# Kernel optimization log

Hardware: AMD Instinct MI355X
Metric: run time of the kernel (lower is better)

Reference implementation:

```python
import jax, jax.numpy as jnp
import numpy as np


def setup_inputs() -> dict:
    key = jax.random.key(0)
    k1, k2 = jax.random.split(key)
    pred = jax.random.normal(k1, (4, 8192, 3), dtype=jnp.float32)
    label = jax.random.normal(k2, (4, 8192, 3), dtype=jnp.float32)
    return {"pred": pred, "label": label}


def reference(pred, label):
    # Pairwise Euclidean distances via the Gram-matrix identity
    # explicit repeat+subtract+norm, without the [B,N,M,D] blowup).
    x2 = jnp.sum(pred * pred, axis=-1)            # [B, N]
    y2 = jnp.sum(label * label, axis=-1)          # [B, M]
    xy = jnp.einsum('bnd,bmd->bnm', pred, label)  # [B, N, M]
    d2 = x2[:, :, None] + y2[:, None, :] - 2.0 * xy
    dis = jnp.sqrt(jnp.maximum(d2, 0.0))          # [B, N, M]
    dis_xy = jnp.mean(jnp.min(dis, axis=2))       # pred -> nearest label
    dis_yx = jnp.mean(jnp.min(dis, axis=1))       # label -> nearest pred
    return dis_xy + dis_yx
```

## Files before the change

### kernel.cpp

```cpp
#include <hip/hip_runtime.h>
#include <math.h>

#define BATCH 4
#define NPTS 8192
#define TPB 256
#define RPT 4
#define ROWS_PER_BLOCK (TPB * RPT)
#define ROW_TILES (NPTS / ROWS_PER_BLOCK)

__global__ __launch_bounds__(TPB) void chamfer_partial(
    const float* __restrict__ pred, const float* __restrict__ label,
    float* __restrict__ ws, int S, int colsPerSeg) {
  const int tid = threadIdx.x;
  const int seg = blockIdx.x % S;
  const int rowTile = blockIdx.x / S;
  const int b = blockIdx.y;
  const int dir = blockIdx.z;
  const float* __restrict__ rows = (dir == 0) ? pred : label;
  const float* __restrict__ cols = (dir == 0) ? label : pred;

  float x0[RPT], x1[RPT], x2[RPT], x2n[RPT], mn[RPT];
  const int rowBase = rowTile * ROWS_PER_BLOCK;
#pragma unroll
  for (int r = 0; r < RPT; ++r) {
    const int row = rowBase + r * TPB + tid;
    const float* p = rows + ((size_t)b * NPTS + row) * 3;
    x0[r] = p[0];
    x1[r] = p[1];
    x2[r] = p[2];
    x2n[r] = x0[r] * x0[r] + x1[r] * x1[r] + x2[r] * x2[r];
    mn[r] = INFINITY;
  }

  __shared__ float4 sh[TPB];
  const int colBase = seg * colsPerSeg;
  for (int c0 = 0; c0 < colsPerSeg; c0 += TPB) {
    __syncthreads();
    {
      const int col = colBase + c0 + tid;
      const float* q = cols + ((size_t)b * NPTS + col) * 3;
      const float y0 = q[0], y1 = q[1], y2 = q[2];
      sh[tid] = make_float4(-2.0f * y0, -2.0f * y1, -2.0f * y2,
                            y0 * y0 + y1 * y1 + y2 * y2);
    }
    __syncthreads();
#pragma unroll 4
    for (int l = 0; l < TPB; l += 2) {
      const float4 ya = sh[l];
      const float4 yb = sh[l + 1];
#pragma unroll
      for (int r = 0; r < RPT; ++r) {
        float ta = fmaf(x0[r], ya.x, ya.w);
        ta = fmaf(x1[r], ya.y, ta);
        ta = fmaf(x2[r], ya.z, ta);
        float tb = fmaf(x0[r], yb.x, yb.w);
        tb = fmaf(x1[r], yb.y, tb);
        tb = fmaf(x2[r], yb.z, tb);
        mn[r] = fminf(mn[r], fminf(ta, tb));
      }
    }
  }

#pragma unroll
  for (int r = 0; r < RPT; ++r) {
    const int row = rowBase + r * TPB + tid;
    ws[(((size_t)dir * BATCH + b) * S + seg) * NPTS + row] = x2n[r] + mn[r];
  }
}

__global__ __launch_bounds__(256) void chamfer_reduce(
    const float* __restrict__ ws, float* __restrict__ out, int S) {
  const int g0 = blockIdx.x * 1024 + threadIdx.x;
  float sum = 0.0f;
#pragma unroll
  for (int k = 0; k < 4; ++k) {
    const int g = g0 + k * 256;
    const int db = g / NPTS;
    const int row = g & (NPTS - 1);
    const float* p = ws + (size_t)db * S * NPTS + row;
    float m = p[0];
    for (int s = 1; s < S; ++s) m = fminf(m, p[(size_t)s * NPTS]);
    m = fmaxf(m, 0.0f);
    sum += sqrtf(m);
  }
  sum *= (1.0f / (float)(BATCH * NPTS));
  for (int off = 32; off > 0; off >>= 1) sum += __shfl_down(sum, off, 64);
  __shared__ float ssum[4];
  const int wid = threadIdx.x >> 6;
  const int lane = threadIdx.x & 63;
  if (lane == 0) ssum[wid] = sum;
  __syncthreads();
  if (threadIdx.x == 0) atomicAdd(out, ssum[0] + ssum[1] + ssum[2] + ssum[3]);
}

extern "C" void kernel_launch(void* const* d_in, const int* in_sizes, int n_in,
                              void* d_out, int out_size, void* d_ws,
                              size_t ws_size, hipStream_t stream) {
  const float* pred = (const float*)d_in[0];
  const float* label = (const float*)d_in[1];
  float* out = (float*)d_out;
  float* ws = (float*)d_ws;

  int S = 16;
  while (S > 1 && (size_t)2 * BATCH * S * NPTS * sizeof(float) > ws_size)
    S >>= 1;
  const int colsPerSeg = NPTS / S;

  hipMemsetAsync(d_out, 0, sizeof(float), stream);

  dim3 grid1(ROW_TILES * S, BATCH, 2);
  chamfer_partial<<<grid1, TPB, 0, stream>>>(pred, label, ws, S, colsPerSeg);
  chamfer_reduce<<<64, 256, 0, stream>>>(ws, out, S);
}
```

Measured before the change: 116.3 us.

## Use v_min3 inline asm, drop memset launch, template reduce on segment count

```diff
diff --git a/kernel.cpp b/kernel.cpp
--- a/kernel.cpp
+++ b/kernel.cpp
@@ -8,9 +8,20 @@
 #define ROWS_PER_BLOCK (TPB * RPT)
 #define ROW_TILES (NPTS / ROWS_PER_BLOCK)
 
-__global__ __launch_bounds__(TPB) void chamfer_partial(
+#define ROW2(mn, x0_, x1_, x2_)                                \
+  do {                                                         \
+    float ta = __builtin_fmaf((x0_), ya.x, ya.w);              \
+    ta = __builtin_fmaf((x1_), ya.y, ta);                      \
+    ta = __builtin_fmaf((x2_), ya.z, ta);                      \
+    float tb = __builtin_fmaf((x0_), yb.x, yb.w);              \
+    tb = __builtin_fmaf((x1_), yb.y, tb);                      \
+    tb = __builtin_fmaf((x2_), yb.z, tb);                      \
+    asm("v_min3_f32 %0, %0, %1, %2" : "+v"(mn) : "v"(ta), "v"(tb)); \
+  } while (0)
+
+__global__ __launch_bounds__(TPB, 4) void chamfer_partial(
     const float* __restrict__ pred, const float* __restrict__ label,
-    float* __restrict__ ws, int S, int colsPerSeg) {
+    float* __restrict__ ws, float* __restrict__ out, int S, int colsPerSeg) {
   const int tid = threadIdx.x;
   const int seg = blockIdx.x % S;
   const int rowTile = blockIdx.x / S;
@@ -19,18 +30,22 @@
   const float* __restrict__ rows = (dir == 0) ? pred : label;
   const float* __restrict__ cols = (dir == 0) ? label : pred;
 
-  float x0[RPT], x1[RPT], x2[RPT], x2n[RPT], mn[RPT];
+  if (blockIdx.x == 0 && b == 0 && dir == 0 && tid == 0) out[0] = 0.0f;
+
   const int rowBase = rowTile * ROWS_PER_BLOCK;
-#pragma unroll
-  for (int r = 0; r < RPT; ++r) {
-    const int row = rowBase + r * TPB + tid;
-    const float* p = rows + ((size_t)b * NPTS + row) * 3;
-    x0[r] = p[0];
-    x1[r] = p[1];
-    x2[r] = p[2];
-    x2n[r] = x0[r] * x0[r] + x1[r] * x1[r] + x2[r] * x2[r];
-    mn[r] = INFINITY;
-  }
+  const float* p0 = rows + ((size_t)b * NPTS + rowBase + 0 * TPB + tid) * 3;
+  const float* p1 = rows + ((size_t)b * NPTS + rowBase + 1 * TPB + tid) * 3;
+  const float* p2 = rows + ((size_t)b * NPTS + rowBase + 2 * TPB + tid) * 3;
+  const float* p3 = rows + ((size_t)b * NPTS + rowBase + 3 * TPB + tid) * 3;
+  const float x00 = p0[0], x01 = p0[1], x02 = p0[2];
+  const float x10 = p1[0], x11 = p1[1], x12 = p1[2];
+  const float x20 = p2[0], x21 = p2[1], x22 = p2[2];
+  const float x30 = p3[0], x31 = p3[1], x32 = p3[2];
+  const float n0 = x00 * x00 + x01 * x01 + x02 * x02;
+  const float n1 = x10 * x10 + x11 * x11 + x12 * x12;
+  const float n2 = x20 * x20 + x21 * x21 + x22 * x22;
+  const float n3 = x30 * x30 + x31 * x31 + x32 * x32;
+  float mn0 = INFINITY, mn1 = INFINITY, mn2 = INFINITY, mn3 = INFINITY;
 
   __shared__ float4 sh[TPB];
   const int colBase = seg * colsPerSeg;
@@ -48,40 +63,35 @@
     for (int l = 0; l < TPB; l += 2) {
       const float4 ya = sh[l];
       const float4 yb = sh[l + 1];
-#pragma unroll
-      for (int r = 0; r < RPT; ++r) {
-        float ta = fmaf(x0[r], ya.x, ya.w);
-        ta = fmaf(x1[r], ya.y, ta);
-        ta = fmaf(x2[r], ya.z, ta);
-        float tb = fmaf(x0[r], yb.x, yb.w);
-        tb = fmaf(x1[r], yb.y, tb);
-        tb = fmaf(x2[r], yb.z, tb);
-        mn[r] = fminf(mn[r], fminf(ta, tb));
-      }
+      ROW2(mn0, x00, x01, x02);
+      ROW2(mn1, x10, x11, x12);
+      ROW2(mn2, x20, x21, x22);
+      ROW2(mn3, x30, x31, x32);
     }
   }
 
-#pragma unroll
-  for (int r = 0; r < RPT; ++r) {
-    const int row = rowBase + r * TPB + tid;
-    ws[(((size_t)dir * BATCH + b) * S + seg) * NPTS + row] = x2n[r] + mn[r];
-  }
+  float* w = ws + (((size_t)dir * BATCH + b) * S + seg) * NPTS + rowBase + tid;
+  w[0 * TPB] = n0 + mn0;
+  w[1 * TPB] = n1 + mn1;
+  w[2 * TPB] = n2 + mn2;
+  w[3 * TPB] = n3 + mn3;
 }
 
+template <int S>
 __global__ __launch_bounds__(256) void chamfer_reduce(
-    const float* __restrict__ ws, float* __restrict__ out, int S) {
+    const float* __restrict__ ws, float* __restrict__ out) {
   const int g0 = blockIdx.x * 1024 + threadIdx.x;
   float sum = 0.0f;
 #pragma unroll
   for (int k = 0; k < 4; ++k) {
     const int g = g0 + k * 256;
-    const int db = g / NPTS;
+    const int db = g >> 13;
     const int row = g & (NPTS - 1);
     const float* p = ws + (size_t)db * S * NPTS + row;
-    float m = p[0];
-    for (int s = 1; s < S; ++s) m = fminf(m, p[(size_t)s * NPTS]);
-    m = fmaxf(m, 0.0f);
-    sum += sqrtf(m);
+    float m = INFINITY;
+#pragma unroll
+    for (int s = 0; s < S; ++s) m = fminf(m, p[(size_t)s * NPTS]);
+    sum += sqrtf(fmaxf(m, 0.0f));
   }
   sum *= (1.0f / (float)(BATCH * NPTS));
   for (int off = 32; off > 0; off >>= 1) sum += __shfl_down(sum, off, 64);
@@ -106,9 +116,14 @@
     S >>= 1;
   const int colsPerSeg = NPTS / S;
 
-  hipMemsetAsync(d_out, 0, sizeof(float), stream);
-
   dim3 grid1(ROW_TILES * S, BATCH, 2);
-  chamfer_partial<<<grid1, TPB, 0, stream>>>(pred, label, ws, S, colsPerSeg);
-  chamfer_reduce<<<64, 256, 0, stream>>>(ws, out, S);
+  chamfer_partial<<<grid1, TPB, 0, stream>>>(pred, label, ws, out, S,
+                                             colsPerSeg);
+  switch (S) {
+    case 16: chamfer_reduce<16><<<64, 256, 0, stream>>>(ws, out); break;
+    case 8:  chamfer_reduce<8><<<64, 256, 0, stream>>>(ws, out); break;
+    case 4:  chamfer_reduce<4><<<64, 256, 0, stream>>>(ws, out); break;
+    case 2:  chamfer_reduce<2><<<64, 256, 0, stream>>>(ws, out); break;
+    default: chamfer_reduce<1><<<64, 256, 0, stream>>>(ws, out); break;
+  }
 }
```

After: 97.69 us. -16.0%, faster.
